# Performance work log

Hardware: AMD Instinct MI355X
Metric: run time of the kernel (lower is better)

Reference implementation:

```python
import jax, jax.numpy as jnp
import numpy as np

EPS_NORM = 1e-6  # MVLayerNorm epsilon


def _build_cayley():
    # Cl(3,0): blades as bitmasks, ordered by (grade, bitmask):
    # [1, e1, e2, e3, e12, e13, e23, e123]
    n = 3
    order = sorted(range(1 << n), key=lambda b: (bin(b).count('1'), b))
    idx = {b: i for i, b in enumerate(order)}
    C = np.zeros((8, 8, 8), dtype=np.float32)
    for a in range(8):
        for b in range(8):
            # sign from reordering basis vectors (Euclidean metric: e_i^2 = +1)
            swaps, ash = 0, a >> 1
            while ash:
                swaps += bin(ash & b).count('1')
                ash >>= 1
            C[idx[a], idx[a ^ b], idx[b]] = -1.0 if swaps % 2 else 1.0
    return C

_CAYLEY_NP = _build_cayley()
CAYLEY = jnp.asarray(_CAYLEY_NP)
# metric of each blade: scalar part of blade*blade -> [1,1,1,1,-1,-1,-1,-1]
METRIC = jnp.asarray(np.array([_CAYLEY_NP[i, 0, i] for i in range(8)], dtype=np.float32))
# blade -> grade subspace index, subspace dims [1,3,3,1]
BLADE2SUB = np.array([0, 1, 1, 1, 2, 2, 2, 3])


def mv_linear(x, w, b):
    # x: (B, in, 8); w: (out, in, 4); b: (out,) added to scalar blade only
    wb = w[:, :, BLADE2SUB]                      # (out, in, 8) per-blade weight
    y = jnp.einsum('bmi,nmi->bni', x, wb)        # (B, out, 8)
    return y.at[..., 0].add(b)


def mv_layernorm(x, a):
    # quadratic form per channel: q = sum_i g_i * x_i^2, shape (B, C, 1)
    q = jnp.einsum('bci,i,bci->bc', x, METRIC, x)[..., None]
    norm = (q * q + 1e-16) ** 0.25               # smooth sqrt(|q|)
    norm = norm.mean(axis=1, keepdims=True) + EPS_NORM  # (B, 1, 1)
    return a[None, :, None] * x / norm


def setup_inputs() -> dict:
    key = jax.random.key(0)
    ks = jax.random.split(key, 8)
    N, C_IN, C_HID, NSUB = 4096, 512, 512, 4
    s = 1.0 / np.sqrt(C_IN)
    return {
        'x': jax.random.normal(ks[0], (N, C_IN, 8), jnp.float32),
        'w1': jax.random.normal(ks[1], (C_HID, C_IN, NSUB), jnp.float32) * s,
        'b1': jax.random.normal(ks[2], (C_HID,), jnp.float32) * 0.02,
        'w2': jax.random.normal(ks[3], (C_HID, C_IN, NSUB), jnp.float32) * s,
        'b2': jax.random.normal(ks[4], (C_HID,), jnp.float32) * 0.02,
        'w3': jax.random.normal(ks[5], (C_IN, C_HID, NSUB), jnp.float32) * s,
        'b3': jax.random.normal(ks[6], (C_IN,), jnp.float32) * 0.02,
        'a_norm': jax.random.normal(ks[7], (C_IN,), jnp.float32) * 0.1 + 1.0,
    }


def reference(x, w1, b1, w2, b2, w3, b3, a_norm):
    x_l = mv_linear(x, w1, b1)                       # (N, hid, 8)
    x_r = mv_linear(x, w2, b2)                       # (N, hid, 8)
    gp = jnp.einsum('bni,ijk,bnk->bnj', x_l, CAYLEY, x_r)  # sparse Cayley product
    y = mv_linear(gp, w3, b3)                        # (N, in, 8)
    return mv_layernorm(y, a_norm)
```

## Files before the change

kernel.cpp:

```cpp
#include <hip/hip_runtime.h>
#include <hip/hip_bf16.h>
#include <cstdint>
#include <cstddef>

typedef __bf16 bf16;
typedef __bf16 bf16x2_t __attribute__((ext_vector_type(2)));
typedef __bf16 bf16x4_t __attribute__((ext_vector_type(4)));
typedef __bf16 bf16x8_t __attribute__((ext_vector_type(8)));
typedef float  f32x2_t  __attribute__((ext_vector_type(2)));
typedef float  f32x4_t  __attribute__((ext_vector_type(4)));

#define NTOK 4096
#define CH   512
#define SLICE (NTOK*CH)
#define WSLICE (CH*CH)

#define AS1 __attribute__((address_space(1)))
#define AS3 __attribute__((address_space(3)))

__device__ __forceinline__ void gl_lds16(const void* g, void* l) {
    __builtin_amdgcn_global_load_lds((const AS1 unsigned int*)g,
                                     (AS3 unsigned int*)l, 16, 0, 0);
}

#define VM_WAIT(N) asm volatile("s_waitcnt vmcnt(" #N ")" ::: "memory")
#define SFENCE()   __builtin_amdgcn_sched_barrier(0)
#define RAW_BAR()  { SFENCE(); __builtin_amdgcn_s_barrier(); SFENCE(); }

__global__ __launch_bounds__(256) void k_convert_x(const float* __restrict__ x,
                                                   bf16* __restrict__ xb) {
    int p = blockIdx.x * 256 + threadIdx.x;
    const f32x4_t* x4 = (const f32x4_t*)x;
    f32x4_t v0 = x4[2*p];
    f32x4_t v1 = x4[2*p+1];
    xb[0*SLICE + p] = (bf16)v0.x;
    xb[1*SLICE + p] = (bf16)v0.y;
    xb[2*SLICE + p] = (bf16)v0.z;
    xb[3*SLICE + p] = (bf16)v0.w;
    xb[4*SLICE + p] = (bf16)v1.x;
    xb[5*SLICE + p] = (bf16)v1.y;
    xb[6*SLICE + p] = (bf16)v1.z;
    xb[7*SLICE + p] = (bf16)v1.w;
}

__global__ __launch_bounds__(256) void k_convert_w(const float* __restrict__ w1,
                                                   const float* __restrict__ w2,
                                                   const float* __restrict__ w3,
                                                   bf16* __restrict__ w1b,
                                                   bf16* __restrict__ w2b,
                                                   bf16* __restrict__ w3b) {
    int p = blockIdx.x * 256 + threadIdx.x;
    const float* w = (blockIdx.y == 0) ? w1 : (blockIdx.y == 1) ? w2 : w3;
    bf16* wb       = (blockIdx.y == 0) ? w1b : (blockIdx.y == 1) ? w2b : w3b;
    f32x4_t v = ((const f32x4_t*)w)[p];
    wb[0*WSLICE + p] = (bf16)v.x;
    wb[1*WSLICE + p] = (bf16)v.y;
    wb[2*WSLICE + p] = (bf16)v.z;
    wb[3*WSLICE + p] = (bf16)v.w;
}

__global__ __launch_bounds__(512, 2) void k_gemm12(const bf16* __restrict__ xb,
                                                   const bf16* __restrict__ w1b,
                                                   const bf16* __restrict__ w2b,
                                                   bf16* __restrict__ xl,
                                                   bf16* __restrict__ xr) {
    const int blade = blockIdx.z;
    const int sub = (blade == 0) ? 0 : (blade < 4) ? 1 : (blade < 7) ? 2 : 3;
    const bf16* A  = xb  + (size_t)blade * SLICE;
    const bf16* B1 = w1b + (size_t)sub * WSLICE;
    const bf16* B2 = w2b + (size_t)sub * WSLICE;
    const int tm = blockIdx.x * 256, tn = blockIdx.y * 128;

    __shared__ __align__(1024) bf16 lsA[2][256 * 64];
    __shared__ __align__(1024) bf16 lsB1[2][128 * 64];
    __shared__ __align__(1024) bf16 lsB2[2][128 * 64];

    const int t = threadIdx.x, lane = t & 63, wid = t >> 6;
    const int waveM = (wid >> 2) * 128, waveN = (wid & 3) * 32;

    const int srow = t >> 3;
    const int sswz = ((t & 7) ^ (srow & 7)) * 8;
    const bf16* Ag  = A  + (size_t)(tm + srow) * CH + sswz;
    const bf16* B1g = B1 + (size_t)(tn + srow) * CH + sswz;
    const bf16* B2g = B2 + (size_t)(tn + srow) * CH + sswz;
    const int wbase = wid * 1024;

    const int xorv  = (lane & 7) << 4;
    const int kbase = (lane >> 4) * 16;

    f32x4_t accL[8][2] = {};
    f32x4_t accR[8][2] = {};

    #define STAGE12(buf, k0) {                                              \
        char* la_  = (char*)lsA[buf]  + wbase;                              \
        char* lb1_ = (char*)lsB1[buf] + wbase;                              \
        char* lb2_ = (char*)lsB2[buf] + wbase;                              \
        _Pragma("unroll")                                                   \
        for (int q = 0; q < 4; ++q)                                         \
            gl_lds16(Ag + (size_t)q * 64 * CH + (k0), la_ + q * 8192);      \
        _Pragma("unroll")                                                   \
        for (int q = 0; q < 2; ++q) {                                       \
            gl_lds16(B1g + (size_t)q * 64 * CH + (k0), lb1_ + q * 8192);    \
            gl_lds16(B2g + (size_t)q * 64 * CH + (k0), lb2_ + q * 8192);    \
        }                                                                   \
    }

    STAGE12(0, 0);
    SFENCE();
    STAGE12(1, 64);
    SFENCE();
    VM_WAIT(8);
    RAW_BAR();

    #pragma unroll 2
    for (int kt = 0; kt < 8; ++kt) {
        const int cur = kt & 1;
        const char* ca  = (const char*)lsA[cur];
        const char* cb1 = (const char*)lsB1[cur];
        const char* cb2 = (const char*)lsB2[cur];
        #pragma unroll
        for (int kk = 0; kk < 2; ++kk) {
            const int koff = kk * 64 + kbase;
            bf16x8_t af[8], b1f[2], b2f[2];
            #pragma unroll
            for (int mf = 0; mf < 8; ++mf) {
                int row = waveM + mf * 16 + (lane & 15);
                af[mf] = *(const bf16x8_t*)(ca + row * 128 + (koff ^ xorv));
            }
            #pragma unroll
            for (int nf = 0; nf < 2; ++nf) {
                int row = waveN + nf * 16 + (lane & 15);
                b1f[nf] = *(const bf16x8_t*)(cb1 + row * 128 + (koff ^ xorv));
                b2f[nf] = *(const bf16x8_t*)(cb2 + row * 128 + (koff ^ xorv));
            }
            __builtin_amdgcn_s_setprio(1);
            #pragma unroll
            for (int mf = 0; mf < 8; ++mf)
                #pragma unroll
                for (int nf = 0; nf < 2; ++nf) {
                    accL[mf][nf] = __builtin_amdgcn_mfma_f32_16x16x32_bf16(
                        b1f[nf], af[mf], accL[mf][nf], 0, 0, 0);
                    accR[mf][nf] = __builtin_amdgcn_mfma_f32_16x16x32_bf16(
                        b2f[nf], af[mf], accR[mf][nf], 0, 0, 0);
                }
            __builtin_amdgcn_s_setprio(0);
            SFENCE();
        }
        RAW_BAR();
        if (kt < 6) {
            STAGE12(cur, (kt + 2) * 64);
            SFENCE();
            VM_WAIT(8);
            RAW_BAR();
        } else if (kt == 6) {
            VM_WAIT(0);
            RAW_BAR();
        }
    }
    #undef STAGE12

    bf16* O1 = xl + (size_t)blade * SLICE;
    bf16* O2 = xr + (size_t)blade * SLICE;
    const int ob  = tm + waveM + (lane & 15);
    const int on0 = tn + waveN + (lane >> 4) * 4;
    #pragma unroll
    for (int mf = 0; mf < 8; ++mf) {
        size_t rowoff = (size_t)(ob + mf * 16) * CH;
        #pragma unroll
        for (int nf = 0; nf < 2; ++nf) {
            bf16x4_t v1, v2;
            #pragma unroll
            for (int r = 0; r < 4; ++r) {
                v1[r] = (bf16)accL[mf][nf][r];
                v2[r] = (bf16)accR[mf][nf][r];
            }
            *(bf16x4_t*)(O1 + rowoff + on0 + nf * 16) = v1;
            *(bf16x4_t*)(O2 + rowoff + on0 + nf * 16) = v2;
        }
    }
}

__global__ __launch_bounds__(512, 2) void k_gemm3(const bf16* __restrict__ gp,
                                                  const bf16* __restrict__ w3b,
                                                  bf16* __restrict__ yb) {
    const int blade = blockIdx.z;
    const int sub = (blade == 0) ? 0 : (blade < 4) ? 1 : (blade < 7) ? 2 : 3;
    const bf16* A = gp  + (size_t)blade * SLICE;
    const bf16* B = w3b + (size_t)sub * WSLICE;
    const int tm = blockIdx.x * 256, tn = blockIdx.y * 256;

    __shared__ __align__(1024) bf16 lsA[2][256 * 64];
    __shared__ __align__(1024) bf16 lsB[2][256 * 64];

    const int t = threadIdx.x, lane = t & 63, wid = t >> 6;
    const int waveM = (wid >> 2) * 128, waveN = (wid & 3) * 64;

    const int srow = t >> 3;
    const int sswz = ((t & 7) ^ (srow & 7)) * 8;
    const bf16* Ag = A + (size_t)(tm + srow) * CH + sswz;
    const bf16* Bg = B + (size_t)(tn + srow) * CH + sswz;
    const int wbase = wid * 1024;

    const int xorv  = (lane & 7) << 4;
    const int kbase = (lane >> 4) * 16;

    f32x4_t acc[8][4] = {};

    #define STAGE3(buf, k0) {                                               \
        char* la_ = (char*)lsA[buf] + wbase;                                \
        char* lb_ = (char*)lsB[buf] + wbase;                                \
        _Pragma("unroll")                                                   \
        for (int q = 0; q < 4; ++q) {                                       \
            gl_lds16(Ag + (size_t)q * 64 * CH + (k0), la_ + q * 8192);      \
            gl_lds16(Bg + (size_t)q * 64 * CH + (k0), lb_ + q * 8192);      \
        }                                                                   \
    }

    STAGE3(0, 0);
    SFENCE();
    STAGE3(1, 64);
    SFENCE();
    VM_WAIT(8);
    RAW_BAR();

    #pragma unroll 2
    for (int kt = 0; kt < 8; ++kt) {
        const int cur = kt & 1;
        const char* ca = (const char*)lsA[cur];
        const char* cb = (const char*)lsB[cur];
        #pragma unroll
        for (int kk = 0; kk < 2; ++kk) {
            const int koff = kk * 64 + kbase;
            bf16x8_t af[8], bf[4];
            #pragma unroll
            for (int mf = 0; mf < 8; ++mf) {
                int row = waveM + mf * 16 + (lane & 15);
                af[mf] = *(const bf16x8_t*)(ca + row * 128 + (koff ^ xorv));
            }
            #pragma unroll
            for (int nf = 0; nf < 4; ++nf) {
                int row = waveN + nf * 16 + (lane & 15);
                bf[nf] = *(const bf16x8_t*)(cb + row * 128 + (koff ^ xorv));
            }
            __builtin_amdgcn_s_setprio(1);
            #pragma unroll
            for (int mf = 0; mf < 8; ++mf)
                #pragma unroll
                for (int nf = 0; nf < 4; ++nf)
                    acc[mf][nf] = __builtin_amdgcn_mfma_f32_16x16x32_bf16(
                        bf[nf], af[mf], acc[mf][nf], 0, 0, 0);
            __builtin_amdgcn_s_setprio(0);
            SFENCE();
        }
        RAW_BAR();
        if (kt < 6) {
            STAGE3(cur, (kt + 2) * 64);
            SFENCE();
            VM_WAIT(8);
            RAW_BAR();
        } else if (kt == 6) {
            VM_WAIT(0);
            RAW_BAR();
        }
    }
    #undef STAGE3

    bf16* O = yb + (size_t)blade * SLICE;
    const int ob  = tm + waveM + (lane & 15);
    const int on0 = tn + waveN + (lane >> 4) * 4;
    #pragma unroll
    for (int mf = 0; mf < 8; ++mf) {
        size_t rowoff = (size_t)(ob + mf * 16) * CH;
        #pragma unroll
        for (int nf = 0; nf < 4; ++nf) {
            bf16x4_t v;
            #pragma unroll
            for (int r = 0; r < 4; ++r) v[r] = (bf16)acc[mf][nf][r];
            *(bf16x4_t*)(O + rowoff + on0 + nf * 16) = v;
        }
    }
}

__global__ __launch_bounds__(256) void k_gp(const bf16* __restrict__ xl,
                                            const bf16* __restrict__ xr,
                                            const float* __restrict__ b1,
                                            const float* __restrict__ b2,
                                            bf16* __restrict__ gp) {
    int p = (blockIdx.x * 256 + threadIdx.x) * 4;
    float l[8][4], r[8][4], g[8][4];
    #pragma unroll
    for (int i = 0; i < 8; ++i) {
        bf16x4_t lv = *(const bf16x4_t*)(xl + (size_t)i * SLICE + p);
        bf16x4_t rv = *(const bf16x4_t*)(xr + (size_t)i * SLICE + p);
        #pragma unroll
        for (int v = 0; v < 4; ++v) { l[i][v] = (float)lv[v]; r[i][v] = (float)rv[v]; g[i][v] = 0.f; }
    }
    int n0 = p & (CH - 1);
    f32x4_t b1v = *(const f32x4_t*)(b1 + n0);
    f32x4_t b2v = *(const f32x4_t*)(b2 + n0);
    #pragma unroll
    for (int v = 0; v < 4; ++v) { l[0][v] += b1v[v]; r[0][v] += b2v[v]; }

    const int IDX[8] = {0, 1, 2, 4, 3, 5, 6, 7};
    #pragma unroll
    for (int a = 0; a < 8; ++a) {
        #pragma unroll
        for (int b = 0; b < 8; ++b) {
            int e = ((((a >> 1) ^ (a >> 2)) & b) & 1) ^ (((a >> 2) & (b >> 1)) & 1);
            int j = IDX[a ^ b], ia = IDX[a], ib = IDX[b];
            #pragma unroll
            for (int v = 0; v < 4; ++v)
                g[j][v] += e ? (-l[ia][v] * r[ib][v]) : (l[ia][v] * r[ib][v]);
        }
    }
    #pragma unroll
    for (int i = 0; i < 8; ++i) {
        bf16x4_t gv;
        #pragma unroll
        for (int v = 0; v < 4; ++v) gv[v] = (bf16)g[i][v];
        *(bf16x4_t*)(gp + (size_t)i * SLICE + p) = gv;
    }
}

__global__ __launch_bounds__(256) void k_ln(const bf16* __restrict__ y,
                                            const float* __restrict__ b3,
                                            const float* __restrict__ an,
                                            float* __restrict__ out) {
    int b = blockIdx.x, t = threadIdx.x;
    int c0 = t * 2;
    size_t base = (size_t)b * CH + c0;
    float yv[2][8];
    #pragma unroll
    for (int i = 0; i < 8; ++i) {
        bf16x2_t v = *(const bf16x2_t*)(y + (size_t)i * SLICE + base);
        yv[0][i] = (float)v[0];
        yv[1][i] = (float)v[1];
    }
    f32x2_t b3v = *(const f32x2_t*)(b3 + c0);
    float nsum = 0.f;
    #pragma unroll
    for (int h = 0; h < 2; ++h) {
        yv[h][0] += b3v[h];
        float q = yv[h][0]*yv[h][0] + yv[h][1]*yv[h][1] + yv[h][2]*yv[h][2] + yv[h][3]*yv[h][3]
                - yv[h][4]*yv[h][4] - yv[h][5]*yv[h][5] - yv[h][6]*yv[h][6] - yv[h][7]*yv[h][7];
        nsum += sqrtf(sqrtf(q * q + 1e-16f));
    }
    #pragma unroll
    for (int off = 32; off; off >>= 1) nsum += __shfl_xor(nsum, off);
    __shared__ float red[4];
    if ((t & 63) == 0) red[t >> 6] = nsum;
    __syncthreads();
    float denom = (red[0] + red[1] + red[2] + red[3]) * (1.f / 512.f) + 1e-6f;
    float inv = 1.f / denom;
    f32x2_t anv = *(const f32x2_t*)(an + c0);
    float out16[16];
    #pragma unroll
    for (int h = 0; h < 2; ++h) {
        float s = anv[h] * inv;
        #pragma unroll
        for (int i = 0; i < 8; ++i) out16[h * 8 + i] = yv[h][i] * s;
    }
    size_t base8 = base * 8;
    #pragma unroll
    for (int j = 0; j < 4; ++j)
        *(f32x4_t*)(out + base8 + j * 4) = *(f32x4_t*)(out16 + j * 4);
}

extern "C" void kernel_launch(void* const* d_in, const int* in_sizes, int n_in,
                              void* d_out, int out_size, void* d_ws, size_t ws_size,
                              hipStream_t stream) {
    (void)in_sizes; (void)n_in; (void)out_size; (void)ws_size;
    const float* x  = (const float*)d_in[0];
    const float* w1 = (const float*)d_in[1];
    const float* b1 = (const float*)d_in[2];
    const float* w2 = (const float*)d_in[3];
    const float* b2 = (const float*)d_in[4];
    const float* w3 = (const float*)d_in[5];
    const float* b3 = (const float*)d_in[6];
    const float* an = (const float*)d_in[7];

    char* ws = (char*)d_ws;
    bf16*  xb  = (bf16*)(ws);
    bf16*  xl  = (bf16*)(ws + 33554432);
    bf16*  xr  = (bf16*)(ws + 67108864);
    bf16*  yb  = (bf16*)(ws + 33554432);
    bf16*  w1b = (bf16*)(ws + 100663296);
    bf16*  w2b = (bf16*)(ws + 102760448);
    bf16*  w3b = (bf16*)(ws + 104857600);

    k_convert_x<<<SLICE / 256, 256, 0, stream>>>(x, xb);
    dim3 gw(WSLICE / 256, 3);
    k_convert_w<<<gw, 256, 0, stream>>>(w1, w2, w3, w1b, w2b, w3b);

    dim3 g12(NTOK / 256, CH / 128, 8);
    k_gemm12<<<g12, 512, 0, stream>>>(xb, w1b, w2b, xl, xr);
    k_gp<<<SLICE / 4 / 256, 256, 0, stream>>>(xl, xr, b1, b2, xb );
    dim3 g3(NTOK / 256, CH / 256, 8);
    k_gemm3<<<g3, 512, 0, stream>>>(xb, w3b, yb);
    k_ln<<<NTOK, 256, 0, stream>>>(yb, b3, an, (float*)d_out);
}
```

Measured before the change: 255.0 us.

## Use smaller GEMM tiles with triple-buffered LDS and a single barrier per k-step

Both GEMM kernels shrink their output tiles: gemm12 goes from 256x128 to 128x128 and gemm3 from 256x256 to 256x128, which doubles the grid size for more parallelism across CUs. Shared memory becomes a three-stage ring, and each iteration issues the global-to-LDS load for stage k+2 before computing stage k. This replaces the two barriers per iteration with one, and the sched_barrier fences are removed. In exchange, each block gets less data reuse, and there is some risk of LDS pressure limiting occupancy.

Result: slower. 260.8 us (+2.3%).

```diff
diff --git a/kernel.cpp b/kernel.cpp
--- a/kernel.cpp
+++ b/kernel.cpp
@@ -24,8 +24,6 @@
 }
 
 #define VM_WAIT(N) asm volatile("s_waitcnt vmcnt(" #N ")" ::: "memory")
-#define SFENCE()   __builtin_amdgcn_sched_barrier(0)
-#define RAW_BAR()  { SFENCE(); __builtin_amdgcn_s_barrier(); SFENCE(); }
 
 __global__ __launch_bounds__(256) void k_convert_x(const float* __restrict__ x,
                                                    bf16* __restrict__ xb) {
@@ -69,14 +67,14 @@
     const bf16* A  = xb  + (size_t)blade * SLICE;
     const bf16* B1 = w1b + (size_t)sub * WSLICE;
     const bf16* B2 = w2b + (size_t)sub * WSLICE;
-    const int tm = blockIdx.x * 256, tn = blockIdx.y * 128;
-
-    __shared__ __align__(1024) bf16 lsA[2][256 * 64];
-    __shared__ __align__(1024) bf16 lsB1[2][128 * 64];
-    __shared__ __align__(1024) bf16 lsB2[2][128 * 64];
+    const int tm = blockIdx.x * 128, tn = blockIdx.y * 128;
+
+    __shared__ __align__(1024) bf16 lsA [3][128 * 64];
+    __shared__ __align__(1024) bf16 lsB1[3][128 * 64];
+    __shared__ __align__(1024) bf16 lsB2[3][128 * 64];
 
     const int t = threadIdx.x, lane = t & 63, wid = t >> 6;
-    const int waveM = (wid >> 2) * 128, waveN = (wid & 3) * 32;
+    const int waveM = (wid >> 2) * 64, waveN = (wid & 3) * 32;
 
     const int srow = t >> 3;
     const int sswz = ((t & 7) ^ (srow & 7)) * 8;
@@ -88,42 +86,39 @@
     const int xorv  = (lane & 7) << 4;
     const int kbase = (lane >> 4) * 16;
 
-    f32x4_t accL[8][2] = {};
-    f32x4_t accR[8][2] = {};
-
-    #define STAGE12(buf, k0) {                                              \
-        char* la_  = (char*)lsA[buf]  + wbase;                              \
-        char* lb1_ = (char*)lsB1[buf] + wbase;                              \
-        char* lb2_ = (char*)lsB2[buf] + wbase;                              \
-        _Pragma("unroll")                                                   \
-        for (int q = 0; q < 4; ++q)                                         \
-            gl_lds16(Ag + (size_t)q * 64 * CH + (k0), la_ + q * 8192);      \
+    f32x4_t accL[4][2] = {};
+    f32x4_t accR[4][2] = {};
+
+    #define STAGE12(s, k0) {                                                \
+        char* la_  = (char*)lsA[s]  + wbase;                                \
+        char* lb1_ = (char*)lsB1[s] + wbase;                                \
+        char* lb2_ = (char*)lsB2[s] + wbase;                                \
         _Pragma("unroll")                                                   \
         for (int q = 0; q < 2; ++q) {                                       \
+            gl_lds16(Ag  + (size_t)q * 64 * CH + (k0), la_  + q * 8192);    \
             gl_lds16(B1g + (size_t)q * 64 * CH + (k0), lb1_ + q * 8192);    \
             gl_lds16(B2g + (size_t)q * 64 * CH + (k0), lb2_ + q * 8192);    \
         }                                                                   \
     }
 
     STAGE12(0, 0);
-    SFENCE();
     STAGE12(1, 64);
-    SFENCE();
-    VM_WAIT(8);
-    RAW_BAR();
-
-    #pragma unroll 2
+    VM_WAIT(6);
+    __builtin_amdgcn_s_barrier();
+
+    #pragma unroll
     for (int kt = 0; kt < 8; ++kt) {
-        const int cur = kt & 1;
+        const int cur = kt % 3;
+        if (kt < 6) STAGE12((kt + 2) % 3, (kt + 2) * 64);
         const char* ca  = (const char*)lsA[cur];
         const char* cb1 = (const char*)lsB1[cur];
         const char* cb2 = (const char*)lsB2[cur];
         #pragma unroll
         for (int kk = 0; kk < 2; ++kk) {
             const int koff = kk * 64 + kbase;
-            bf16x8_t af[8], b1f[2], b2f[2];
-            #pragma unroll
-            for (int mf = 0; mf < 8; ++mf) {
+            bf16x8_t af[4], b1f[2], b2f[2];
+            #pragma unroll
+            for (int mf = 0; mf < 4; ++mf) {
                 int row = waveM + mf * 16 + (lane & 15);
                 af[mf] = *(const bf16x8_t*)(ca + row * 128 + (koff ^ xorv));
             }
@@ -135,7 +130,7 @@
             }
             __builtin_amdgcn_s_setprio(1);
             #pragma unroll
-            for (int mf = 0; mf < 8; ++mf)
+            for (int mf = 0; mf < 4; ++mf)
                 #pragma unroll
                 for (int nf = 0; nf < 2; ++nf) {
                     accL[mf][nf] = __builtin_amdgcn_mfma_f32_16x16x32_bf16(
@@ -144,18 +139,10 @@
                         b2f[nf], af[mf], accR[mf][nf], 0, 0, 0);
                 }
             __builtin_amdgcn_s_setprio(0);
-            SFENCE();
-        }
-        RAW_BAR();
-        if (kt < 6) {
-            STAGE12(cur, (kt + 2) * 64);
-            SFENCE();
-            VM_WAIT(8);
-            RAW_BAR();
-        } else if (kt == 6) {
-            VM_WAIT(0);
-            RAW_BAR();
-        }
+        }
+        if (kt < 6)      VM_WAIT(6);
+        else if (kt == 6) VM_WAIT(0);
+        if (kt < 7) __builtin_amdgcn_s_barrier();
     }
     #undef STAGE12
 
@@ -164,7 +151,7 @@
     const int ob  = tm + waveM + (lane & 15);
     const int on0 = tn + waveN + (lane >> 4) * 4;
     #pragma unroll
-    for (int mf = 0; mf < 8; ++mf) {
+    for (int mf = 0; mf < 4; ++mf) {
         size_t rowoff = (size_t)(ob + mf * 16) * CH;
         #pragma unroll
         for (int nf = 0; nf < 2; ++nf) {
@@ -187,13 +174,13 @@
     const int sub = (blade == 0) ? 0 : (blade < 4) ? 1 : (blade < 7) ? 2 : 3;
     const bf16* A = gp  + (size_t)blade * SLICE;
     const bf16* B = w3b + (size_t)sub * WSLICE;
-    const int tm = blockIdx.x * 256, tn = blockIdx.y * 256;
-
-    __shared__ __align__(1024) bf16 lsA[2][256 * 64];
-    __shared__ __align__(1024) bf16 lsB[2][256 * 64];
+    const int tm = blockIdx.x * 256, tn = blockIdx.y * 128;
+
+    __shared__ __align__(1024) bf16 lsA[3][256 * 64];
+    __shared__ __align__(1024) bf16 lsB[3][128 * 64];
 
     const int t = threadIdx.x, lane = t & 63, wid = t >> 6;
-    const int waveM = (wid >> 2) * 128, waveN = (wid & 3) * 64;
+    const int waveM = (wid >> 2) * 128, waveN = (wid & 3) * 32;
 
     const int srow = t >> 3;
     const int sswz = ((t & 7) ^ (srow & 7)) * 8;
@@ -204,41 +191,41 @@
     const int xorv  = (lane & 7) << 4;
     const int kbase = (lane >> 4) * 16;
 
-    f32x4_t acc[8][4] = {};
-
-    #define STAGE3(buf, k0) {                                               \
-        char* la_ = (char*)lsA[buf] + wbase;                                \
-        char* lb_ = (char*)lsB[buf] + wbase;                                \
+    f32x4_t acc[8][2] = {};
+
+    #define STAGE3(s, k0) {                                                 \
+        char* la_ = (char*)lsA[s] + wbase;                                  \
+        char* lb_ = (char*)lsB[s] + wbase;                                  \
         _Pragma("unroll")                                                   \
-        for (int q = 0; q < 4; ++q) {                                       \
+        for (int q = 0; q < 4; ++q)                                         \
             gl_lds16(Ag + (size_t)q * 64 * CH + (k0), la_ + q * 8192);      \
+        _Pragma("unroll")                                                   \
+        for (int q = 0; q < 2; ++q)                                         \
             gl_lds16(Bg + (size_t)q * 64 * CH + (k0), lb_ + q * 8192);      \
-        }                                                                   \
     }
 
     STAGE3(0, 0);
-    SFENCE();
     STAGE3(1, 64);
-    SFENCE();
-    VM_WAIT(8);
-    RAW_BAR();
-
-    #pragma unroll 2
+    VM_WAIT(6);
+    __builtin_amdgcn_s_barrier();
+
+    #pragma unroll
     for (int kt = 0; kt < 8; ++kt) {
-        const int cur = kt & 1;
+        const int cur = kt % 3;
+        if (kt < 6) STAGE3((kt + 2) % 3, (kt + 2) * 64);
         const char* ca = (const char*)lsA[cur];
         const char* cb = (const char*)lsB[cur];
         #pragma unroll
         for (int kk = 0; kk < 2; ++kk) {
             const int koff = kk * 64 + kbase;
-            bf16x8_t af[8], bf[4];
+            bf16x8_t af[8], bf[2];
             #pragma unroll
             for (int mf = 0; mf < 8; ++mf) {
                 int row = waveM + mf * 16 + (lane & 15);
                 af[mf] = *(const bf16x8_t*)(ca + row * 128 + (koff ^ xorv));
             }
             #pragma unroll
-            for (int nf = 0; nf < 4; ++nf) {
+            for (int nf = 0; nf < 2; ++nf) {
                 int row = waveN + nf * 16 + (lane & 15);
                 bf[nf] = *(const bf16x8_t*)(cb + row * 128 + (koff ^ xorv));
             }
@@ -246,22 +233,14 @@
             #pragma unroll
             for (int mf = 0; mf < 8; ++mf)
                 #pragma unroll
-                for (int nf = 0; nf < 4; ++nf)
+                for (int nf = 0; nf < 2; ++nf)
                     acc[mf][nf] = __builtin_amdgcn_mfma_f32_16x16x32_bf16(
                         bf[nf], af[mf], acc[mf][nf], 0, 0, 0);
             __builtin_amdgcn_s_setprio(0);
-            SFENCE();
-        }
-        RAW_BAR();
-        if (kt < 6) {
-            STAGE3(cur, (kt + 2) * 64);
-            SFENCE();
-            VM_WAIT(8);
-            RAW_BAR();
-        } else if (kt == 6) {
-            VM_WAIT(0);
-            RAW_BAR();
-        }
+        }
+        if (kt < 6)      VM_WAIT(6);
+        else if (kt == 6) VM_WAIT(0);
+        if (kt < 7) __builtin_amdgcn_s_barrier();
     }
     #undef STAGE3
 
@@ -272,7 +251,7 @@
     for (int mf = 0; mf < 8; ++mf) {
         size_t rowoff = (size_t)(ob + mf * 16) * CH;
         #pragma unroll
-        for (int nf = 0; nf < 4; ++nf) {
+        for (int nf = 0; nf < 2; ++nf) {
             bf16x4_t v;
             #pragma unroll
             for (int r = 0; r < 4; ++r) v[r] = (bf16)acc[mf][nf][r];
@@ -392,10 +371,10 @@
     dim3 gw(WSLICE / 256, 3);
     k_convert_w<<<gw, 256, 0, stream>>>(w1, w2, w3, w1b, w2b, w3b);
 
-    dim3 g12(NTOK / 256, CH / 128, 8);
+    dim3 g12(NTOK / 128, CH / 128, 8);
     k_gemm12<<<g12, 512, 0, stream>>>(xb, w1b, w2b, xl, xr);
     k_gp<<<SLICE / 4 / 256, 256, 0, stream>>>(xl, xr, b1, b2, xb );
-    dim3 g3(NTOK / 256, CH / 256, 8);
+    dim3 g3(NTOK / 256, CH / 128, 8);
     k_gemm3<<<g3, 512, 0, stream>>>(xb, w3b, yb);
     k_ln<<<NTOK, 256, 0, stream>>>(yb, b3, an, (float*)d_out);
 }
```
